# Kernel tuning notes

Hardware: AMD Instinct MI355X
Metric: run time of the kernel (lower is better)

Reference implementation:

```python
import jax, jax.numpy as jnp
import numpy as np

N_NODES = 100000
N_EDGES = 1600000
IN_FEATS = 128
N_HIDDEN = 128
N_CLASSES = 64


def setup_inputs() -> dict:
    key = jax.random.key(0)
    ks = jax.random.split(key, 12)
    features = jax.random.normal(ks[0], (N_NODES, IN_FEATS), dtype=jnp.float32)
    src = jax.random.randint(ks[1], (N_EDGES,), 0, N_NODES, dtype=jnp.int32)
    dst = jax.random.randint(ks[2], (N_EDGES,), 0, N_NODES, dtype=jnp.int32)
    def lin(k, fi, fo):
        s = 1.0 / np.sqrt(fi)
        kw, kb = jax.random.split(k)
        W = jax.random.uniform(kw, (fi, fo), jnp.float32, -s, s)
        b = jax.random.uniform(kb, (fo,), jnp.float32, -s, s)
        return W, b
    W1, b1 = lin(ks[3], IN_FEATS, N_HIDDEN)
    W2a, b2a = lin(ks[4], N_HIDDEN, N_HIDDEN)
    W2b, b2b = lin(ks[5], N_HIDDEN, N_HIDDEN)
    W3, b3 = lin(ks[6], N_HIDDEN, N_CLASSES)
    eps = jnp.zeros((4,), jnp.float32)  # learnable eps, one per GINConv
    return dict(features=features, src=src, dst=dst, W1=W1, b1=b1,
                W2a=W2a, b2a=b2a, W2b=W2b, b2b=b2b, W3=W3, b3=b3, eps=eps)


def _aggregate(h, src, dst, mode, deg):
    # messages flow src -> dst; h[src] is [E, d]
    msg = h[src]
    if mode == 'sum':
        return jax.ops.segment_sum(msg, dst, num_segments=N_NODES)
    if mode == 'mean':
        s = jax.ops.segment_sum(msg, dst, num_segments=N_NODES)
        return s / jnp.maximum(deg, 1.0)[:, None]
    # max: DGL yields 0 for nodes with no incoming edges
    m = jax.ops.segment_max(msg, dst, num_segments=N_NODES)
    return jnp.where(deg[:, None] > 0, m, 0.0)


def reference(features, src, dst, W1, b1, W2a, b2a, W2b, b2b, W3, b3, eps):
    deg = jax.ops.segment_sum(jnp.ones((N_EDGES,), jnp.float32), dst,
                              num_segments=N_NODES)
    h = features
    # layer 0: max aggregation + Linear + ReLU (dropout = identity in eval)
    h = (1.0 + eps[0]) * h + _aggregate(h, src, dst, 'max', deg)
    h = jax.nn.relu(h @ W1 + b1)
    # middle layers: sum aggregation + Linear + ReLU
    h = (1.0 + eps[1]) * h + _aggregate(h, src, dst, 'sum', deg)
    h = jax.nn.relu(h @ W2a + b2a)
    h = (1.0 + eps[2]) * h + _aggregate(h, src, dst, 'sum', deg)
    h = jax.nn.relu(h @ W2b + b2b)
    # output layer: mean aggregation + Linear (no activation)
    h = (1.0 + eps[3]) * h + _aggregate(h, src, dst, 'mean', deg)
    h = h @ W3 + b3
    return h
```

## Files before the change

kernel.cpp:

```cpp
#include <hip/hip_runtime.h>
#include <math.h>

#define N_NODES 100000
#define N_EDGES 1600000
#define FEAT 128
#define NBUCKET 391
#define BCAP 5120

typedef __attribute__((ext_vector_type(8))) _Float16 half8;
typedef __attribute__((ext_vector_type(4))) float floatx4;

__device__ inline half8 h8max(half8 a, half8 b) {
    return __builtin_elementwise_max(a, b);
}

__global__ __launch_bounds__(256) void prep_all(const float* __restrict__ feat,
                                                _Float16* __restrict__ featH,
                                                const float* __restrict__ W1,
                                                const float* __restrict__ W2a,
                                                const float* __restrict__ W2b,
                                                const float* __restrict__ W3,
                                                _Float16* __restrict__ WT1,
                                                _Float16* __restrict__ WT2a,
                                                _Float16* __restrict__ WT2b,
                                                _Float16* __restrict__ WT3,
                                                int* __restrict__ gcur) {
    const int n4 = (N_NODES * FEAT) / 4;
    int idx = blockIdx.x * 256 + threadIdx.x;
    if (idx < n4) {
        float4 v = ((const float4*)feat)[idx];
        union { uint2 u; _Float16 h[4]; } p;
        p.h[0] = (_Float16)v.x; p.h[1] = (_Float16)v.y;
        p.h[2] = (_Float16)v.z; p.h[3] = (_Float16)v.w;
        *(uint2*)(featH + 4 * (size_t)idx) = p.u;
        return;
    }
    int off = idx - n4;
    if (off < 16384) { int n = off / 128, k = off % 128; WT1[off] = (_Float16)W1[k * 128 + n]; return; }
    off -= 16384;
    if (off < 16384) { int n = off / 128, k = off % 128; WT2a[off] = (_Float16)W2a[k * 128 + n]; return; }
    off -= 16384;
    if (off < 16384) { int n = off / 128, k = off % 128; WT2b[off] = (_Float16)W2b[k * 128 + n]; return; }
    off -= 16384;
    if (off < 8192)  { int n = off / 128, k = off % 128; WT3[off] = (_Float16)W3[k * 64 + n]; return; }
    off -= 8192;
    if (off < NBUCKET) gcur[off] = 0;
}

__global__ __launch_bounds__(512) void bin_edges(const int* __restrict__ src,
                                                 const int* __restrict__ dst,
                                                 uint2* __restrict__ ebuf,
                                                 int* __restrict__ gcur) {
    __shared__ int hist[NBUCKET];
    __shared__ int lbase[NBUCKET];
    __shared__ int cur[NBUCKET];
    __shared__ uint2 tile[4096];

    int t = threadIdx.x;
    int e0 = blockIdx.x * 4096;
    for (int i = t; i < NBUCKET; i += 512) { hist[i] = 0; cur[i] = 0; }
    __syncthreads();

    for (int i = t; i < 4096; i += 512) {
        int e = e0 + i;
        uint2 v; v.x = 0u; v.y = 0xffffffffu;
        if (e < N_EDGES) { v.x = (unsigned)src[e]; v.y = (unsigned)dst[e]; }
        tile[i] = v;
        if (v.y != 0xffffffffu) atomicAdd(&hist[v.y >> 8], 1);
    }
    __syncthreads();

    for (int i = t; i < NBUCKET; i += 512) {
        int c = hist[i];
        lbase[i] = (c > 0) ? atomicAdd(&gcur[i], c) : 0;
    }
    __syncthreads();

    for (int i = t; i < 4096; i += 512) {
        uint2 v = tile[i];
        if (v.y == 0xffffffffu) continue;
        int b = (int)(v.y >> 8);
        int p = lbase[b] + atomicAdd(&cur[b], 1);
        if (p < BCAP) ebuf[(size_t)b * BCAP + p] = v;
    }
}

__global__ __launch_bounds__(512) void scan_buckets(const int* __restrict__ gcur,
                                                    int* __restrict__ bbase,
                                                    int* __restrict__ rowptr) {
    __shared__ int s[512];
    int t = threadIdx.x;
    int v = (t < NBUCKET) ? gcur[t] : 0;
    s[t] = v;
    __syncthreads();
    for (int off = 1; off < 512; off <<= 1) {
        int u = (t >= off) ? s[t - off] : 0;
        __syncthreads();
        s[t] += u;
        __syncthreads();
    }
    if (t < NBUCKET) bbase[t] = s[t] - v;
    if (t == 0) rowptr[N_NODES] = N_EDGES;
}

__global__ __launch_bounds__(256) void bucket_csr(const uint2* __restrict__ ebuf,
                                                  const int* __restrict__ gcur,
                                                  const int* __restrict__ bbase,
                                                  int* __restrict__ rowptr,
                                                  int* __restrict__ esrc) {
    __shared__ int cnt[256];
    __shared__ int off[256];
    __shared__ int astart[256];
    __shared__ int cur[256];

    int b = blockIdx.x, t = threadIdx.x;
    int total = gcur[b]; if (total > BCAP) total = BCAP;
    int base = bbase[b];
    const uint2* eb = ebuf + (size_t)b * BCAP;

    cnt[t] = 0; cur[t] = 0;
    __syncthreads();
    for (int i = t; i < total; i += 256) atomicAdd(&cnt[eb[i].y & 255], 1);
    __syncthreads();

    int v = cnt[t];
    off[t] = v;
    __syncthreads();
    for (int o = 1; o < 256; o <<= 1) {
        int u = (t >= o) ? off[t - o] : 0;
        __syncthreads();
        off[t] += u;
        __syncthreads();
    }
    int excl = off[t] - v;
    int node = (b << 8) + t;
    if (node < N_NODES) rowptr[node] = base + excl;
    astart[t] = base + excl;
    __syncthreads();

    for (int i = t; i < total; i += 256) {
        uint2 e = eb[i];
        int ln = (int)(e.y & 255);
        int p = astart[ln] + atomicAdd(&cur[ln], 1);
        esrc[p] = (int)e.x;
    }
}

template <int MODE, int D, bool OUTF32, bool BIAS>
__global__ __launch_bounds__(256) void agg_kernel(const _Float16* __restrict__ h,
                                                  const int* __restrict__ rowptr,
                                                  const int* __restrict__ esrc,
                                                  const float* __restrict__ eps,
                                                  int ei,
                                                  const float* __restrict__ bias,
                                                  _Float16* __restrict__ outH,
                                                  float* __restrict__ outF) {
    constexpr int LPE = D / 8;
    constexpr int NPW = 64 / LPE;
    int wid = (int)((blockIdx.x * 256 + threadIdx.x) >> 6);
    int l = threadIdx.x & 63;
    int grp = l / LPE, sl = l % LPE;
    int node = wid * NPW + grp;
    if (node >= N_NODES) return;
    int beg = rowptr[node], end = rowptr[node + 1];
    int deg = end - beg;

    const _Float16 NEUT = (MODE == 0) ? (_Float16)(-65504.0f) : (_Float16)(0.0f);
    half8 neut8 = {NEUT, NEUT, NEUT, NEUT, NEUT, NEUT, NEUT, NEUT};
    half8 acc = neut8;

    for (int e = beg; e < end; e += 8) {
        half8 v[8];
#pragma unroll
        for (int j = 0; j < 8; ++j) {
            int ee = e + j;
            int s = esrc[ee < end ? ee : end - 1];
            v[j] = *(const half8*)(h + (size_t)s * D + sl * 8);
        }
#pragma unroll
        for (int j = 0; j < 8; ++j)
            if (e + j >= end) v[j] = neut8;
        if (MODE == 0) {
            half8 m01 = h8max(v[0], v[1]), m23 = h8max(v[2], v[3]);
            half8 m45 = h8max(v[4], v[5]), m67 = h8max(v[6], v[7]);
            acc = h8max(acc, h8max(h8max(m01, m23), h8max(m45, m67)));
        } else {
            half8 s01 = v[0] + v[1], s23 = v[2] + v[3];
            half8 s45 = v[4] + v[5], s67 = v[6] + v[7];
            acc += (s01 + s23) + (s45 + s67);
        }
    }

    float a[8];
#pragma unroll
    for (int i = 0; i < 8; ++i) a[i] = (float)acc[i];
    if (MODE == 0 && deg == 0) {
#pragma unroll
        for (int i = 0; i < 8; ++i) a[i] = 0.f;
    }
    if (MODE == 2) {
        float inv = 1.f / (float)(deg > 0 ? deg : 1);
#pragma unroll
        for (int i = 0; i < 8; ++i) a[i] *= inv;
    }
    float sc = 1.f + eps[ei];
    half8 self = *(const half8*)(h + (size_t)node * D + sl * 8);
    float o[8];
#pragma unroll
    for (int i = 0; i < 8; ++i) o[i] = fmaf(sc, (float)self[i], a[i]);

    if (OUTF32) {
#pragma unroll
        for (int i = 0; i < 8; ++i)
            if (BIAS) o[i] += bias[sl * 8 + i];
        float4* dstp = (float4*)(outF + (size_t)node * D + sl * 8);
        dstp[0] = make_float4(o[0], o[1], o[2], o[3]);
        dstp[1] = make_float4(o[4], o[5], o[6], o[7]);
    } else {
        half8 ov;
#pragma unroll
        for (int i = 0; i < 8; ++i) ov[i] = (_Float16)o[i];
        *(half8*)(outH + (size_t)node * D + sl * 8) = ov;
    }
}

template <int BN, bool RELU, bool BIAS>
__global__ __launch_bounds__(256) void gemm_mfma(const _Float16* __restrict__ X,
                                                 const _Float16* __restrict__ WT,
                                                 const float* __restrict__ bias,
                                                 _Float16* __restrict__ Yh) {
    __shared__ _Float16 Ws[BN * 128];
    char* wb = (char*)Ws;

    int t = threadIdx.x;
    int l = t & 63, w = t >> 6;
    int lr = l & 15, lg = l >> 4;
    int rowBase = blockIdx.x * 64;

#pragma unroll
    for (int p = 0; p < BN / 16; ++p) {
        int idx = p * 4096 + t * 16;
        int row = idx >> 8, byte = idx & 255;
        *(half8*)(wb + row * 256 + (byte ^ ((row & 7) << 4))) =
            *(const half8*)((const char*)WT + idx);
    }
    __syncthreads();

    constexpr int NCT = BN / 16;
    floatx4 acc[NCT];
#pragma unroll
    for (int ct = 0; ct < NCT; ++ct)
#pragma unroll
        for (int r = 0; r < 4; ++r) acc[ct][r] = 0.f;

    int grow = rowBase + w * 16 + lr;
    int arow = grow < N_NODES ? grow : 0;
    const char* xrow = (const char*)(X + (size_t)arow * 128);

#pragma unroll
    for (int ks = 0; ks < 4; ++ks) {
        half8 a = *(const half8*)(xrow + ks * 64 + lg * 16);
#pragma unroll
        for (int ct = 0; ct < NCT; ++ct) {
            int n = ct * 16 + lr;
            half8 b = *(const half8*)(wb + n * 256 + ((ks * 64 + lg * 16) ^ ((n & 7) << 4)));
            acc[ct] = __builtin_amdgcn_mfma_f32_16x16x32_f16(a, b, acc[ct], 0, 0, 0);
        }
    }

    float bv[NCT];
#pragma unroll
    for (int ct = 0; ct < NCT; ++ct) bv[ct] = BIAS ? bias[ct * 16 + lr] : 0.f;

    constexpr int ROWB = BN * 2;
    __syncthreads();
#pragma unroll
    for (int ct = 0; ct < NCT; ++ct)
#pragma unroll
        for (int r = 0; r < 4; ++r) {
            int row = w * 16 + lg * 4 + r;
            int col = ct * 16 + lr;
            float v = acc[ct][r] + bv[ct];
            if (RELU) v = fmaxf(v, 0.f);
            *(_Float16*)(wb + row * ROWB + ((col * 2) ^ ((row & 7) << 4))) =
                (_Float16)v;
        }
    __syncthreads();
    {
        int row = t >> 2, q = t & 3;
        int g2 = rowBase + row;
        if (g2 < N_NODES) {
            char* dstp = (char*)(Yh + (size_t)g2 * BN) + q * (ROWB / 4);
#pragma unroll
            for (int j = 0; j < ROWB / 64; ++j) {
                int byte = q * (ROWB / 4) + j * 16;
                half8 v = *(const half8*)(wb + row * ROWB + (byte ^ ((row & 7) << 4)));
                *(half8*)(dstp + j * 16) = v;
            }
        }
    }
}

extern "C" void kernel_launch(void* const* d_in, const int* in_sizes, int n_in,
                              void* d_out, int out_size, void* d_ws, size_t ws_size,
                              hipStream_t stream) {
    const float* feat = (const float*)d_in[0];
    const int*   src  = (const int*)d_in[1];
    const int*   dst  = (const int*)d_in[2];
    const float* W1   = (const float*)d_in[3];
    const float* b1   = (const float*)d_in[4];
    const float* W2a  = (const float*)d_in[5];
    const float* b2a  = (const float*)d_in[6];
    const float* W2b  = (const float*)d_in[7];
    const float* b2b  = (const float*)d_in[8];
    const float* W3   = (const float*)d_in[9];
    const float* b3   = (const float*)d_in[10];
    const float* eps  = (const float*)d_in[11];

    const size_t NH = (size_t)N_NODES * FEAT;
    char* base = (char*)d_ws;
    auto alloc = [&](size_t bytes) {
        char* p = base;
        base += (bytes + 255) & ~(size_t)255;
        return p;
    };
    _Float16* featH = (_Float16*)alloc(NH * 2);
    _Float16* hA    = (_Float16*)alloc(NH * 2);
    _Float16* hB    = (_Float16*)alloc(NH * 2);
    _Float16* WT1   = (_Float16*)alloc(128 * 128 * 2);
    _Float16* WT2a  = (_Float16*)alloc(128 * 128 * 2);
    _Float16* WT2b  = (_Float16*)alloc(128 * 128 * 2);
    _Float16* WT3   = (_Float16*)alloc(128 * 64 * 2);
    uint2* ebuf     = (uint2*)alloc((size_t)NBUCKET * BCAP * 8);
    int* rowptr     = (int*)alloc((N_NODES + 1) * 4);
    int* esrc       = (int*)alloc((size_t)N_EDGES * 4);
    int* gcur       = (int*)alloc(NBUCKET * 4);
    int* bbase      = (int*)alloc(NBUCKET * 4);

    const int PREP_ITEMS = (int)(NH / 4) + 16384 * 3 + 8192 + NBUCKET;
    prep_all<<<(PREP_ITEMS + 255) / 256, 256, 0, stream>>>(
        feat, featH, W1, W2a, W2b, W3, WT1, WT2a, WT2b, WT3, gcur);

    bin_edges<<<(N_EDGES + 4095) / 4096, 512, 0, stream>>>(src, dst, ebuf, gcur);
    scan_buckets<<<1, 512, 0, stream>>>(gcur, bbase, rowptr);
    bucket_csr<<<NBUCKET, 256, 0, stream>>>(ebuf, gcur, bbase, rowptr, esrc);

    const int AGG128_GRID = (N_NODES + 15) / 16;
    const int AGG64_GRID  = (N_NODES + 31) / 32;
    const int GEMM_GRID   = (N_NODES + 63) / 64;

    agg_kernel<0, 128, false, false><<<AGG128_GRID, 256, 0, stream>>>(
        featH, rowptr, esrc, eps, 0, nullptr, hB, nullptr);
    gemm_mfma<128, true, true><<<GEMM_GRID, 256, 0, stream>>>(hB, WT1, b1, hA);
    agg_kernel<1, 128, false, false><<<AGG128_GRID, 256, 0, stream>>>(
        hA, rowptr, esrc, eps, 1, nullptr, hB, nullptr);
    gemm_mfma<128, true, true><<<GEMM_GRID, 256, 0, stream>>>(hB, WT2a, b2a, hA);
    agg_kernel<1, 128, false, false><<<AGG128_GRID, 256, 0, stream>>>(
        hA, rowptr, esrc, eps, 2, nullptr, hB, nullptr);
    gemm_mfma<128, true, true><<<GEMM_GRID, 256, 0, stream>>>(hB, WT2b, b2b, hA);
    gemm_mfma<64, false, false><<<GEMM_GRID, 256, 0, stream>>>(hA, WT3, nullptr, hB);
    agg_kernel<2, 64, true, true><<<AGG64_GRID, 256, 0, stream>>>(
        hB, rowptr, esrc, eps, 3, b3, nullptr, (float*)d_out);
}
```

Baseline: 325.6 us.

## Double GEMM rows per block and add nontemporal load/store hints

The MFMA GEMM now covers 128 rows per block: each wave computes two 16-row tiles against the same shared-memory weight fragments, which halves the weight staging per row and halves the grid. Separately, nontemporal hints are added to the feature conversion loads, the esrc index loads and the output stores in the aggregation kernels, and the GEMM activation loads. The hints aim to cut cache pollution from streaming traffic. They risk evicting data the next kernel re-reads, such as esrc, which is reused across layers, and the aggregation outputs consumed by the following GEMM.

```diff
diff --git a/kernel.cpp b/kernel.cpp
--- a/kernel.cpp
+++ b/kernel.cpp
@@ -12,6 +12,12 @@
 
 __device__ inline half8 h8max(half8 a, half8 b) {
     return __builtin_elementwise_max(a, b);
+}
+__device__ inline half8 nt_load_h8(const _Float16* p) {
+    return __builtin_nontemporal_load((const half8*)p);
+}
+__device__ inline void nt_store_h8(_Float16* p, half8 v) {
+    __builtin_nontemporal_store(v, (half8*)p);
 }
 
 __global__ __launch_bounds__(256) void prep_all(const float* __restrict__ feat,
@@ -28,7 +34,7 @@
     const int n4 = (N_NODES * FEAT) / 4;
     int idx = blockIdx.x * 256 + threadIdx.x;
     if (idx < n4) {
-        float4 v = ((const float4*)feat)[idx];
+        floatx4 v = __builtin_nontemporal_load((const floatx4*)feat + idx);
         union { uint2 u; _Float16 h[4]; } p;
         p.h[0] = (_Float16)v.x; p.h[1] = (_Float16)v.y;
         p.h[2] = (_Float16)v.z; p.h[3] = (_Float16)v.w;
@@ -174,7 +180,7 @@
 #pragma unroll
         for (int j = 0; j < 8; ++j) {
             int ee = e + j;
-            int s = esrc[ee < end ? ee : end - 1];
+            int s = __builtin_nontemporal_load(&esrc[ee < end ? ee : end - 1]);
             v[j] = *(const half8*)(h + (size_t)s * D + sl * 8);
         }
 #pragma unroll
@@ -213,14 +219,16 @@
 #pragma unroll
         for (int i = 0; i < 8; ++i)
             if (BIAS) o[i] += bias[sl * 8 + i];
-        float4* dstp = (float4*)(outF + (size_t)node * D + sl * 8);
-        dstp[0] = make_float4(o[0], o[1], o[2], o[3]);
-        dstp[1] = make_float4(o[4], o[5], o[6], o[7]);
+        floatx4* dstp = (floatx4*)(outF + (size_t)node * D + sl * 8);
+        floatx4 o0 = {o[0], o[1], o[2], o[3]};
+        floatx4 o1 = {o[4], o[5], o[6], o[7]};
+        __builtin_nontemporal_store(o0, dstp);
+        __builtin_nontemporal_store(o1, dstp + 1);
     } else {
         half8 ov;
 #pragma unroll
         for (int i = 0; i < 8; ++i) ov[i] = (_Float16)o[i];
-        *(half8*)(outH + (size_t)node * D + sl * 8) = ov;
+        nt_store_h8(outH + (size_t)node * D + sl * 8, ov);
     }
 }
 
@@ -235,7 +243,7 @@
     int t = threadIdx.x;
     int l = t & 63, w = t >> 6;
     int lr = l & 15, lg = l >> 4;
-    int rowBase = blockIdx.x * 64;
+    int rowBase = blockIdx.x * 128;
 
 #pragma unroll
     for (int p = 0; p < BN / 16; ++p) {
@@ -247,24 +255,33 @@
     __syncthreads();
 
     constexpr int NCT = BN / 16;
-    floatx4 acc[NCT];
-#pragma unroll
-    for (int ct = 0; ct < NCT; ++ct)
-#pragma unroll
-        for (int r = 0; r < 4; ++r) acc[ct][r] = 0.f;
-
-    int grow = rowBase + w * 16 + lr;
-    int arow = grow < N_NODES ? grow : 0;
-    const char* xrow = (const char*)(X + (size_t)arow * 128);
+    floatx4 acc[2][NCT];
+#pragma unroll
+    for (int rt = 0; rt < 2; ++rt)
+#pragma unroll
+        for (int ct = 0; ct < NCT; ++ct)
+#pragma unroll
+            for (int r = 0; r < 4; ++r) acc[rt][ct][r] = 0.f;
+
+    const _Float16* xrow[2];
+#pragma unroll
+    for (int rt = 0; rt < 2; ++rt) {
+        int grow = rowBase + w * 32 + rt * 16 + lr;
+        xrow[rt] = X + (size_t)(grow < N_NODES ? grow : 0) * 128;
+    }
 
 #pragma unroll
     for (int ks = 0; ks < 4; ++ks) {
-        half8 a = *(const half8*)(xrow + ks * 64 + lg * 16);
+        half8 a[2];
+#pragma unroll
+        for (int rt = 0; rt < 2; ++rt)
+            a[rt] = nt_load_h8(xrow[rt] + ks * 32 + lg * 8);
 #pragma unroll
         for (int ct = 0; ct < NCT; ++ct) {
             int n = ct * 16 + lr;
             half8 b = *(const half8*)(wb + n * 256 + ((ks * 64 + lg * 16) ^ ((n & 7) << 4)));
-            acc[ct] = __builtin_amdgcn_mfma_f32_16x16x32_f16(a, b, acc[ct], 0, 0, 0);
+            acc[0][ct] = __builtin_amdgcn_mfma_f32_16x16x32_f16(a[0], b, acc[0][ct], 0, 0, 0);
+            acc[1][ct] = __builtin_amdgcn_mfma_f32_16x16x32_f16(a[1], b, acc[1][ct], 0, 0, 0);
         }
     }
 
@@ -275,25 +292,27 @@
     constexpr int ROWB = BN * 2;
     __syncthreads();
 #pragma unroll
-    for (int ct = 0; ct < NCT; ++ct)
-#pragma unroll
-        for (int r = 0; r < 4; ++r) {
-            int row = w * 16 + lg * 4 + r;
-            int col = ct * 16 + lr;
-            float v = acc[ct][r] + bv[ct];
-            if (RELU) v = fmaxf(v, 0.f);
-            *(_Float16*)(wb + row * ROWB + ((col * 2) ^ ((row & 7) << 4))) =
-                (_Float16)v;
-        }
+    for (int rt = 0; rt < 2; ++rt)
+#pragma unroll
+        for (int ct = 0; ct < NCT; ++ct)
+#pragma unroll
+            for (int r = 0; r < 4; ++r) {
+                int row = w * 32 + rt * 16 + lg * 4 + r;
+                int col = ct * 16 + lr;
+                float v = acc[rt][ct][r] + bv[ct];
+                if (RELU) v = fmaxf(v, 0.f);
+                *(_Float16*)(wb + row * ROWB + ((col * 2) ^ ((row & 7) << 4))) =
+                    (_Float16)v;
+            }
     __syncthreads();
     {
-        int row = t >> 2, q = t & 3;
+        int row = t >> 1, hf = t & 1;
         int g2 = rowBase + row;
         if (g2 < N_NODES) {
-            char* dstp = (char*)(Yh + (size_t)g2 * BN) + q * (ROWB / 4);
-#pragma unroll
-            for (int j = 0; j < ROWB / 64; ++j) {
-                int byte = q * (ROWB / 4) + j * 16;
+            char* dstp = (char*)(Yh + (size_t)g2 * BN) + hf * (ROWB / 2);
+#pragma unroll
+            for (int j = 0; j < ROWB / 32; ++j) {
+                int byte = hf * (ROWB / 2) + j * 16;
                 half8 v = *(const half8*)(wb + row * ROWB + (byte ^ ((row & 7) << 4)));
                 *(half8*)(dstp + j * 16) = v;
             }
@@ -347,7 +366,7 @@
 
     const int AGG128_GRID = (N_NODES + 15) / 16;
     const int AGG64_GRID  = (N_NODES + 31) / 32;
-    const int GEMM_GRID   = (N_NODES + 63) / 64;
+    const int GEMM_GRID   = (N_NODES + 127) / 128;
 
     agg_kernel<0, 128, false, false><<<AGG128_GRID, 256, 0, stream>>>(
         featH, rowptr, esrc, eps, 0, nullptr, hB, nullptr);
```

Measured after the change: 353.1 us. 8.5% more time.
